# Performance work log

Hardware: AMD Instinct MI355X
Metric: run time of the kernel (lower is better)

The kernel has to match this reference:

```python
import jax, jax.numpy as jnp
import numpy as np

B, T, C = 2, 2048, 1024
N_HEAD = 16
HEAD_DIM = C // N_HEAD


def setup_inputs() -> dict:
    key = jax.random.key(0)
    ks = jax.random.split(key, 5)
    s = 0.02
    return {
        "x": jax.random.normal(ks[0], (B, T, C), dtype=jnp.float32),
        "Wq": jax.random.normal(ks[1], (C, C), dtype=jnp.float32) * s,
        "bq": jnp.zeros((C,), dtype=jnp.float32),
        "Wk": jax.random.normal(ks[2], (C, C), dtype=jnp.float32) * s,
        "bk": jnp.zeros((C,), dtype=jnp.float32),
        "Wv": jax.random.normal(ks[3], (C, C), dtype=jnp.float32) * s,
        "bv": jnp.zeros((C,), dtype=jnp.float32),
        "Wo": jax.random.normal(ks[4], (C, C), dtype=jnp.float32) * s,
        "bo": jnp.zeros((C,), dtype=jnp.float32),
    }


def reference(x, Wq, bq, Wk, bk, Wv, bv, Wo, bo):
    b, t, c = x.shape
    h, d = N_HEAD, HEAD_DIM
    # projections -> [B, H, T, D]
    def proj(W, bias):
        return (x @ W.T + bias).reshape(b, t, h, d).transpose(0, 2, 1, 3)
    q = proj(Wq, bq)
    k = proj(Wk, bk)
    v = proj(Wv, bv)
    att = jnp.einsum("bhqd,bhkd->bhqk", q, k) / jnp.sqrt(jnp.float32(d))
    causal = jnp.tril(jnp.ones((t, t), dtype=bool))
    att = jnp.where(causal, att, jnp.float32(-jnp.inf))
    att = jax.nn.softmax(att, axis=-1)
    y = jnp.einsum("bhqk,bhkd->bhqd", att, v)  # [B,H,T,D]
    y = y.transpose(0, 2, 1, 3).reshape(b, t, c)
    return y @ Wo.T + bo
```

## Files before the change

kernel.cpp:

```cpp
#include <hip/hip_runtime.h>
#include <hip/hip_bf16.h>


namespace {

constexpr int TT = 2048;
constexpr int CC = 1024;
constexpr int HH = 16;
constexpr int DD = 64;

using bf16x8 = __attribute__((ext_vector_type(8))) __bf16;
using bf16x4 = __attribute__((ext_vector_type(4))) __bf16;
using f32x4  = __attribute__((ext_vector_type(4))) float;
using us8    = __attribute__((ext_vector_type(8))) unsigned short;

__device__ __forceinline__ unsigned short f2b(float f) {
  unsigned u = __float_as_uint(f);
  u += 0x7fffu + ((u >> 16) & 1u);
  return (unsigned short)(u >> 16);
}

__device__ __forceinline__ void gload16(const void* g, void* l) {
  __builtin_amdgcn_global_load_lds(
      (const __attribute__((address_space(1))) void*)g,
      (__attribute__((address_space(3))) void*)l, 16, 0, 0);
}

#if __has_builtin(__builtin_amdgcn_exp2f)
#define FEXP2 __builtin_amdgcn_exp2f
#else
#define FEXP2 exp2f
#endif

#define SCALE2 0.18033688011112042f

}

__global__ void k_cvt_all(const float* __restrict__ x,
                          const float* __restrict__ wq, const float* __restrict__ wk,
                          const float* __restrict__ wv, const float* __restrict__ wo,
                          unsigned short* __restrict__ dst) {
  const int i = blockIdx.x * 256 + threadIdx.x;
  const float* src; int off;
  if (i < 1048576)      { src = x;  off = i; }
  else if (i < 1310720) { src = wq; off = i - 1048576; }
  else if (i < 1572864) { src = wk; off = i - 1310720; }
  else if (i < 1835008) { src = wv; off = i - 1572864; }
  else                  { src = wo; off = i - 1835008; }
  float4 v = reinterpret_cast<const float4*>(src)[off];
  ushort4 o;
  o.x = f2b(v.x); o.y = f2b(v.y); o.z = f2b(v.z); o.w = f2b(v.w);
  reinterpret_cast<ushort4*>(dst)[i] = o;
}

__global__ __launch_bounds__(256, 3) void k_gemm_qkv(
    const unsigned short* __restrict__ A,
    const unsigned short* __restrict__ Wq,
    const unsigned short* __restrict__ Wk,
    const unsigned short* __restrict__ Wv,
    const float* __restrict__ bq,
    const float* __restrict__ bk,
    const float* __restrict__ bv,
    unsigned short* __restrict__ qd,
    unsigned short* __restrict__ kd,
    unsigned short* __restrict__ vd)
{
  __shared__ unsigned short la[2][128 * 32];
  __shared__ unsigned short lb[2][128 * 32];
  const int tid = threadIdx.x;
  const int lane = tid & 63;
  const int wid = tid >> 6;
  const int l15 = lane & 15, lg = lane >> 4;
  const int wm = (wid & 1) * 64, wn = (wid >> 1) * 64;
  const int bm = blockIdx.x;
  const int wsel = blockIdx.y >> 3;
  const int bnl = blockIdx.y & 7;

  const unsigned short* W = (wsel == 0) ? Wq : (wsel == 1) ? Wk : Wv;
  const float* bias = (wsel == 0) ? bq : (wsel == 1) ? bk : bv;

  const int srow = lane >> 2;
  const int sko  = (lane & 3) * 8;

  auto STAGE = [&](int buf, int kt) {
#pragma unroll
    for (int s = 0; s < 2; ++s) {
      const int seg = wid * 2 + s;
      const int row = seg * 16 + srow;
      gload16(&A[(bm * 128 + row) * CC + kt * 32 + sko], &la[buf][seg * 512]);
      gload16(&W[(bnl * 128 + row) * CC + kt * 32 + sko], &lb[buf][seg * 512]);
    }
  };

  f32x4 acc[4][4];
#pragma unroll
  for (int i = 0; i < 4; ++i)
#pragma unroll
    for (int j = 0; j < 4; ++j) acc[i][j] = f32x4{0.f, 0.f, 0.f, 0.f};

  auto COMPUTE = [&](int buf) {
    bf16x8 af[4], bf[4];
#pragma unroll
    for (int mi = 0; mi < 4; ++mi)
      af[mi] = __builtin_bit_cast(bf16x8,
        *reinterpret_cast<const us8*>(&la[buf][(wm + mi * 16 + l15) * 32 + lg * 8]));
#pragma unroll
    for (int ni = 0; ni < 4; ++ni)
      bf[ni] = __builtin_bit_cast(bf16x8,
        *reinterpret_cast<const us8*>(&lb[buf][(wn + ni * 16 + l15) * 32 + lg * 8]));
#pragma unroll
    for (int mi = 0; mi < 4; ++mi)
#pragma unroll
      for (int ni = 0; ni < 4; ++ni)
        acc[mi][ni] = __builtin_amdgcn_mfma_f32_16x16x32_bf16(af[mi], bf[ni], acc[mi][ni], 0, 0, 0);
  };

  STAGE(0, 0);
  STAGE(1, 1);
  int cur = 0;
  for (int kt = 0; kt < CC / 32 - 1; ++kt) {
    asm volatile("s_waitcnt vmcnt(4)" ::: "memory");
    __builtin_amdgcn_s_barrier();
    COMPUTE(cur);
    __builtin_amdgcn_s_barrier();
    if (kt < CC / 32 - 2) STAGE(cur, kt + 2);
    cur ^= 1;
  }
  asm volatile("s_waitcnt vmcnt(0)" ::: "memory");
  __builtin_amdgcn_s_barrier();
  COMPUTE(cur);

#pragma unroll
  for (int ni = 0; ni < 4; ++ni) {
    const int nl = bnl * 128 + wn + ni * 16 + l15;
    const float bvl = bias[nl];
    const int hh = nl >> 6, d = nl & (DD - 1);
#pragma unroll
    for (int mi = 0; mi < 4; ++mi) {
#pragma unroll
      for (int r = 0; r < 4; ++r) {
        const int m = bm * 128 + wm + mi * 16 + lg * 4 + r;
        const unsigned short bb = f2b(acc[mi][ni][r] + bvl);
        const int b = m >> 11, t = m & (TT - 1);
        if (wsel == 0)
          qd[((b * HH + hh) * TT + t) * DD + d] = bb;
        else if (wsel == 1)
          kd[((b * HH + hh) * TT + t) * DD + d] = bb;
        else
          vd[((b * HH + hh) * DD + d) * TT + t] = bb;
      }
    }
  }
}

__global__ __launch_bounds__(256, 2) void k_gemm_o(
    const unsigned short* __restrict__ A,
    const unsigned short* __restrict__ W,
    const float* __restrict__ bias,
    float* __restrict__ out)
{
  __shared__ unsigned short la[2][128 * 32];
  __shared__ unsigned short lb[2][64 * 32];
  const int tid = threadIdx.x;
  const int lane = tid & 63;
  const int wid = tid >> 6;
  const int l15 = lane & 15, lg = lane >> 4;
  const int wm = (wid & 1) * 64, wn = (wid >> 1) * 32;
  const int bm = blockIdx.x, bn = blockIdx.y;

  const int srow = lane >> 2;
  const int sko  = (lane & 3) * 8;

  auto STAGE = [&](int buf, int kt) {
#pragma unroll
    for (int s = 0; s < 2; ++s) {
      const int seg = wid * 2 + s;
      gload16(&A[(bm * 128 + seg * 16 + srow) * CC + kt * 32 + sko], &la[buf][seg * 512]);
    }
    gload16(&W[(bn * 64 + wid * 16 + srow) * CC + kt * 32 + sko], &lb[buf][wid * 512]);
  };

  f32x4 acc[4][2];
#pragma unroll
  for (int i = 0; i < 4; ++i)
#pragma unroll
    for (int j = 0; j < 2; ++j) acc[i][j] = f32x4{0.f, 0.f, 0.f, 0.f};

  auto COMPUTE = [&](int buf) {
    bf16x8 af[4], bf[2];
#pragma unroll
    for (int mi = 0; mi < 4; ++mi)
      af[mi] = __builtin_bit_cast(bf16x8,
        *reinterpret_cast<const us8*>(&la[buf][(wm + mi * 16 + l15) * 32 + lg * 8]));
#pragma unroll
    for (int ni = 0; ni < 2; ++ni)
      bf[ni] = __builtin_bit_cast(bf16x8,
        *reinterpret_cast<const us8*>(&lb[buf][(wn + ni * 16 + l15) * 32 + lg * 8]));
#pragma unroll
    for (int mi = 0; mi < 4; ++mi)
#pragma unroll
      for (int ni = 0; ni < 2; ++ni)
        acc[mi][ni] = __builtin_amdgcn_mfma_f32_16x16x32_bf16(af[mi], bf[ni], acc[mi][ni], 0, 0, 0);
  };

  STAGE(0, 0);
  STAGE(1, 1);
  int cur = 0;
  for (int kt = 0; kt < CC / 32 - 1; ++kt) {
    asm volatile("s_waitcnt vmcnt(3)" ::: "memory");
    __builtin_amdgcn_s_barrier();
    COMPUTE(cur);
    __builtin_amdgcn_s_barrier();
    if (kt < CC / 32 - 2) STAGE(cur, kt + 2);
    cur ^= 1;
  }
  asm volatile("s_waitcnt vmcnt(0)" ::: "memory");
  __builtin_amdgcn_s_barrier();
  COMPUTE(cur);

#pragma unroll
  for (int ni = 0; ni < 2; ++ni) {
    const int n = bn * 64 + wn + ni * 16 + l15;
    const float bvl = bias[n];
#pragma unroll
    for (int mi = 0; mi < 4; ++mi)
#pragma unroll
      for (int r = 0; r < 4; ++r) {
        const int m = bm * 128 + wm + mi * 16 + lg * 4 + r;
        out[m * CC + n] = acc[mi][ni][r] + bvl;
      }
  }
}

__global__ __launch_bounds__(64) void k_attn(
    const unsigned short* __restrict__ Q,
    const unsigned short* __restrict__ K,
    const unsigned short* __restrict__ VT,
    unsigned short* __restrict__ Y)
{
  __shared__ unsigned short pl[2][2][16][80];
  const int lane = threadIdx.x;
  const int l15 = lane & 15, lg = lane >> 4;
  const int wg = blockIdx.x + 32 * blockIdx.y;
  const int swz = (wg & 7) * 128 + (wg >> 3);
  const int p = swz & 31;
  const int bh = swz >> 5;
  const int b = bh >> 4, h = bh & 15;
  const int qb0A = p * 32;
  const int qb0B = (63 - p) * 32;
  const int nktA = (qb0A + 95) >> 6;
  const int nktB = (qb0B + 95) >> 6;

  const unsigned short* Qh = Q + bh * TT * DD;
  const unsigned short* Kh = K + bh * TT * DD;
  const unsigned short* Vh = VT + bh * DD * TT;

  auto ldq = [&](bf16x8 (&qf)[2][2], int qb0) {
#pragma unroll
    for (int qi = 0; qi < 2; ++qi)
#pragma unroll
      for (int kk = 0; kk < 2; ++kk)
        qf[qi][kk] = __builtin_bit_cast(bf16x8,
          *reinterpret_cast<const us8*>(&Qh[(qb0 + qi * 16 + l15) * DD + kk * 32 + lg * 8]));
  };
  auto ldk = [&](bf16x8 (&kf)[4][2], int kb) {
#pragma unroll
    for (int f = 0; f < 4; ++f)
#pragma unroll
      for (int kk = 0; kk < 2; ++kk)
        kf[f][kk] = __builtin_bit_cast(bf16x8,
          *reinterpret_cast<const us8*>(&Kh[(kb + f * 16 + l15) * DD + kk * 32 + lg * 8]));
  };
  auto ldv = [&](bf16x8 (&vf)[2][4], int kb) {
#pragma unroll
    for (int kk = 0; kk < 2; ++kk)
#pragma unroll
      for (int dc = 0; dc < 4; ++dc)
        vf[kk][dc] = __builtin_bit_cast(bf16x8,
          *reinterpret_cast<const us8*>(&Vh[(dc * 16 + l15) * TT + kb + kk * 32 + lg * 8]));
  };

  bf16x8 qfA[2][2], qfB[2][2];
  ldq(qfA, qb0A); ldq(qfB, qb0B);

  f32x4 oA[2][4], oB[2][4];
  float mrA[2], lrA[2], mrB[2], lrB[2];
#pragma unroll
  for (int qi = 0; qi < 2; ++qi) {
    mrA[qi] = -INFINITY; lrA[qi] = 0.f;
    mrB[qi] = -INFINITY; lrB[qi] = 0.f;
#pragma unroll
    for (int dc = 0; dc < 4; ++dc) {
      oA[qi][dc] = f32x4{0.f, 0.f, 0.f, 0.f};
      oB[qi][dc] = f32x4{0.f, 0.f, 0.f, 0.f};
    }
  }

  auto processSet = [&](const int qb0, const bf16x8 (&qf)[2][2], f32x4 (&o)[2][4],
                        float (&mr)[2], float (&lr)[2],
                        unsigned short (&plS)[2][16][80],
                        const bf16x8 (&kf)[4][2], const bf16x8 (&vf)[2][4],
                        const int kbase) {
    f32x4 s[2][4];
#pragma unroll
    for (int qi = 0; qi < 2; ++qi)
#pragma unroll
      for (int f = 0; f < 4; ++f) {
        f32x4 t0 = __builtin_amdgcn_mfma_f32_16x16x32_bf16(kf[f][0], qf[qi][0],
                                                           f32x4{0.f,0.f,0.f,0.f}, 0, 0, 0);
        s[qi][f] = __builtin_amdgcn_mfma_f32_16x16x32_bf16(kf[f][1], qf[qi][1], t0, 0, 0, 0);
      }
    const bool needMask = (kbase + 63 > qb0);
#pragma unroll
    for (int qi = 0; qi < 2; ++qi) {
      const int qg = qb0 + qi * 16 + l15;
      float sv[4][4];
      float mt = -INFINITY;
#pragma unroll
      for (int f = 0; f < 4; ++f)
#pragma unroll
        for (int r = 0; r < 4; ++r) {
          float v = s[qi][f][r] * SCALE2;
          if (needMask) v = (kbase + f * 16 + lg * 4 + r <= qg) ? v : -INFINITY;
          sv[f][r] = v;
          mt = fmaxf(mt, v);
        }
      mt = fmaxf(mt, __shfl_xor(mt, 16));
      mt = fmaxf(mt, __shfl_xor(mt, 32));
      const float mn = fmaxf(mr[qi], mt);
      const float al = FEXP2(mr[qi] - mn);
      mr[qi] = mn;
      float rs = 0.f;
#pragma unroll
      for (int f = 0; f < 4; ++f) {
        const float p0 = FEXP2(sv[f][0] - mn), p1 = FEXP2(sv[f][1] - mn);
        const float p2 = FEXP2(sv[f][2] - mn), p3 = FEXP2(sv[f][3] - mn);
        rs += (p0 + p1) + (p2 + p3);
        bf16x4 pk;
        pk[0] = (__bf16)p0; pk[1] = (__bf16)p1; pk[2] = (__bf16)p2; pk[3] = (__bf16)p3;
        *reinterpret_cast<bf16x4*>(&plS[qi][l15][f * 16 + lg * 4]) = pk;
      }
      rs += __shfl_xor(rs, 16);
      rs += __shfl_xor(rs, 32);
      lr[qi] = lr[qi] * al + rs;
      float alr[4];
#pragma unroll
      for (int r = 0; r < 4; ++r) alr[r] = __shfl(al, lg * 4 + r);
#pragma unroll
      for (int dc = 0; dc < 4; ++dc)
#pragma unroll
        for (int r = 0; r < 4; ++r) o[qi][dc][r] *= alr[r];
    }
    asm volatile("s_waitcnt lgkmcnt(0)" ::: "memory");
    __builtin_amdgcn_sched_barrier(0);
#pragma unroll
    for (int qi = 0; qi < 2; ++qi) {
      const bf16x8 pa0 = __builtin_bit_cast(bf16x8,
        *reinterpret_cast<const us8*>(&plS[qi][l15][lg * 8]));
      const bf16x8 pa1 = __builtin_bit_cast(bf16x8,
        *reinterpret_cast<const us8*>(&plS[qi][l15][32 + lg * 8]));
#pragma unroll
      for (int dc = 0; dc < 4; ++dc) {
        o[qi][dc] = __builtin_amdgcn_mfma_f32_16x16x32_bf16(pa0, vf[0][dc], o[qi][dc], 0, 0, 0);
        o[qi][dc] = __builtin_amdgcn_mfma_f32_16x16x32_bf16(pa1, vf[1][dc], o[qi][dc], 0, 0, 0);
      }
    }
  };

  bf16x8 kf0[4][2], kf1[4][2];
  ldk(kf0, 0);
  for (int kt = 0; kt < nktB; kt += 2) {
    bf16x8 vf0[2][4];
    ldv(vf0, kt * 64);
    const int nx1 = (kt + 1 < nktB) ? kt + 1 : nktB - 1;
    ldk(kf1, nx1 * 64);
    processSet(qb0B, qfB, oB, mrB, lrB, pl[0], kf0, vf0, kt * 64);
    if (kt < nktA)
      processSet(qb0A, qfA, oA, mrA, lrA, pl[1], kf0, vf0, kt * 64);
    if (kt + 1 < nktB) {
      bf16x8 vf1[2][4];
      ldv(vf1, (kt + 1) * 64);
      const int nx2 = (kt + 2 < nktB) ? kt + 2 : nktB - 1;
      ldk(kf0, nx2 * 64);
      processSet(qb0B, qfB, oB, mrB, lrB, pl[0], kf1, vf1, (kt + 1) * 64);
      if (kt + 1 < nktA)
        processSet(qb0A, qfA, oA, mrA, lrA, pl[1], kf1, vf1, (kt + 1) * 64);
    }
  }

  auto epi = [&](int qb0, f32x4 (&o)[2][4], float (&lr)[2]) {
#pragma unroll
    for (int qi = 0; qi < 2; ++qi) {
      float linv[4];
#pragma unroll
      for (int r = 0; r < 4; ++r) linv[r] = 1.f / __shfl(lr[qi], lg * 4 + r);
#pragma unroll
      for (int r = 0; r < 4; ++r) {
        const int t = qb0 + qi * 16 + lg * 4 + r;
#pragma unroll
        for (int dc = 0; dc < 4; ++dc)
          Y[(b * TT + t) * CC + h * DD + dc * 16 + l15] = f2b(o[qi][dc][r] * linv[r]);
      }
    }
  };
  epi(qb0B, oB, lrB);
  epi(qb0A, oA, lrA);
}

extern "C" void kernel_launch(void* const* d_in, const int* in_sizes, int n_in,
                              void* d_out, int out_size, void* d_ws, size_t ws_size,
                              hipStream_t stream) {
  const float* x  = (const float*)d_in[0];
  const float* Wq = (const float*)d_in[1];
  const float* bq = (const float*)d_in[2];
  const float* Wk = (const float*)d_in[3];
  const float* bk = (const float*)d_in[4];
  const float* Wv = (const float*)d_in[5];
  const float* bv = (const float*)d_in[6];
  const float* Wo = (const float*)d_in[7];
  const float* bo = (const float*)d_in[8];
  float* out = (float*)d_out;

  unsigned short* ws  = (unsigned short*)d_ws;
  unsigned short* xb  = ws;
  unsigned short* wqb = xb  + 4194304;
  unsigned short* wkb = wqb + 1048576;
  unsigned short* wvb = wkb + 1048576;
  unsigned short* wob = wvb + 1048576;
  unsigned short* qb  = wob + 1048576;
  unsigned short* kb  = qb  + 4194304;
  unsigned short* vt  = kb  + 4194304;
  unsigned short* yb  = xb;

  k_cvt_all<<<8192, 256, 0, stream>>>(x, Wq, Wk, Wv, Wo, ws);

  k_gemm_qkv<<<dim3(32, 24), 256, 0, stream>>>(xb, wqb, wkb, wvb, bq, bk, bv, qb, kb, vt);

  k_attn<<<dim3(32, 32), 64, 0, stream>>>(qb, kb, vt, yb);

  k_gemm_o<<<dim3(32, 16), 256, 0, stream>>>(yb, wob, bo, out);
}
```

Measured before the change: 205.3 us.

## Fold softmax scale into Q projection and transpose PV MFMA operand order

Folds the attention scale into the Q projection epilogue, so the per-score multiply in the softmax is gone. Swaps the operands of the P·V MFMA so the output accumulator is laid out with the query row per lane. This removes the shuffles that broadcast alpha and l, and lets the epilogue write packed bf16x4 stores. It also drops the manual double-buffered K prefetch in favour of a simple per-tile load loop, which may expose more global-load latency.

```diff
diff --git a/kernel.cpp b/kernel.cpp
--- a/kernel.cpp
+++ b/kernel.cpp
@@ -140,7 +140,9 @@
 #pragma unroll
       for (int r = 0; r < 4; ++r) {
         const int m = bm * 128 + wm + mi * 16 + lg * 4 + r;
-        const unsigned short bb = f2b(acc[mi][ni][r] + bvl);
+        float val = acc[mi][ni][r] + bvl;
+        if (wsel == 0) val *= SCALE2;
+        const unsigned short bb = f2b(val);
         const int b = m >> 11, t = m & (TT - 1);
         if (wsel == 0)
           qd[((b * HH + hh) * TT + t) * DD + d] = bb;
@@ -263,22 +265,6 @@
         qf[qi][kk] = __builtin_bit_cast(bf16x8,
           *reinterpret_cast<const us8*>(&Qh[(qb0 + qi * 16 + l15) * DD + kk * 32 + lg * 8]));
   };
-  auto ldk = [&](bf16x8 (&kf)[4][2], int kb) {
-#pragma unroll
-    for (int f = 0; f < 4; ++f)
-#pragma unroll
-      for (int kk = 0; kk < 2; ++kk)
-        kf[f][kk] = __builtin_bit_cast(bf16x8,
-          *reinterpret_cast<const us8*>(&Kh[(kb + f * 16 + l15) * DD + kk * 32 + lg * 8]));
-  };
-  auto ldv = [&](bf16x8 (&vf)[2][4], int kb) {
-#pragma unroll
-    for (int kk = 0; kk < 2; ++kk)
-#pragma unroll
-      for (int dc = 0; dc < 4; ++dc)
-        vf[kk][dc] = __builtin_bit_cast(bf16x8,
-          *reinterpret_cast<const us8*>(&Vh[(dc * 16 + l15) * TT + kb + kk * 32 + lg * 8]));
-  };
 
   bf16x8 qfA[2][2], qfB[2][2];
   ldq(qfA, qb0A); ldq(qfB, qb0B);
@@ -296,110 +282,112 @@
     }
   }
 
-  auto processSet = [&](const int qb0, const bf16x8 (&qf)[2][2], f32x4 (&o)[2][4],
-                        float (&mr)[2], float (&lr)[2],
-                        unsigned short (&plS)[2][16][80],
-                        const bf16x8 (&kf)[4][2], const bf16x8 (&vf)[2][4],
-                        const int kbase) {
-    f32x4 s[2][4];
-#pragma unroll
-    for (int qi = 0; qi < 2; ++qi)
-#pragma unroll
-      for (int f = 0; f < 4; ++f) {
-        f32x4 t0 = __builtin_amdgcn_mfma_f32_16x16x32_bf16(kf[f][0], qf[qi][0],
-                                                           f32x4{0.f,0.f,0.f,0.f}, 0, 0, 0);
-        s[qi][f] = __builtin_amdgcn_mfma_f32_16x16x32_bf16(kf[f][1], qf[qi][1], t0, 0, 0, 0);
+  for (int kt = 0; kt < nktB; ++kt) {
+    const int kbase = kt * 64;
+    bf16x8 kf[4][2], vf[2][4];
+#pragma unroll
+    for (int f = 0; f < 4; ++f)
+#pragma unroll
+      for (int kk = 0; kk < 2; ++kk)
+        kf[f][kk] = __builtin_bit_cast(bf16x8,
+          *reinterpret_cast<const us8*>(&Kh[(kbase + f * 16 + l15) * DD + kk * 32 + lg * 8]));
+#pragma unroll
+    for (int kk = 0; kk < 2; ++kk)
+#pragma unroll
+      for (int dc = 0; dc < 4; ++dc)
+        vf[kk][dc] = __builtin_bit_cast(bf16x8,
+          *reinterpret_cast<const us8*>(&Vh[(dc * 16 + l15) * TT + kbase + kk * 32 + lg * 8]));
+
+    const bool doA = (kt < nktA);
+
+    auto qk_sm = [&](const bf16x8 (&qf)[2][2], const int qb0, float (&mr)[2],
+                     float (&lr)[2], f32x4 (&o)[2][4],
+                     unsigned short (&plS)[2][16][80]) {
+      f32x4 s[2][4];
+#pragma unroll
+      for (int qi = 0; qi < 2; ++qi)
+#pragma unroll
+        for (int f = 0; f < 4; ++f) {
+          f32x4 t0 = __builtin_amdgcn_mfma_f32_16x16x32_bf16(kf[f][0], qf[qi][0],
+                                                             f32x4{0.f,0.f,0.f,0.f}, 0, 0, 0);
+          s[qi][f] = __builtin_amdgcn_mfma_f32_16x16x32_bf16(kf[f][1], qf[qi][1], t0, 0, 0, 0);
+        }
+      const bool needMask = (kbase + 63 > qb0);
+#pragma unroll
+      for (int qi = 0; qi < 2; ++qi) {
+        const int qg = qb0 + qi * 16 + l15;
+        float mt = -INFINITY;
+#pragma unroll
+        for (int f = 0; f < 4; ++f)
+#pragma unroll
+          for (int r = 0; r < 4; ++r) {
+            float v = s[qi][f][r];
+            if (needMask) v = (kbase + f * 16 + lg * 4 + r <= qg) ? v : -INFINITY;
+            s[qi][f][r] = v;
+            mt = fmaxf(mt, v);
+          }
+        mt = fmaxf(mt, __shfl_xor(mt, 16));
+        mt = fmaxf(mt, __shfl_xor(mt, 32));
+        const float mn = fmaxf(mr[qi], mt);
+        const float al = FEXP2(mr[qi] - mn);
+        mr[qi] = mn;
+        float rs = 0.f;
+#pragma unroll
+        for (int f = 0; f < 4; ++f) {
+          const float p0 = FEXP2(s[qi][f][0] - mn), p1 = FEXP2(s[qi][f][1] - mn);
+          const float p2 = FEXP2(s[qi][f][2] - mn), p3 = FEXP2(s[qi][f][3] - mn);
+          rs += (p0 + p1) + (p2 + p3);
+          bf16x4 pk;
+          pk[0] = (__bf16)p0; pk[1] = (__bf16)p1; pk[2] = (__bf16)p2; pk[3] = (__bf16)p3;
+          *reinterpret_cast<bf16x4*>(&plS[qi][l15][f * 16 + lg * 4]) = pk;
+        }
+        rs += __shfl_xor(rs, 16);
+        rs += __shfl_xor(rs, 32);
+        lr[qi] = lr[qi] * al + rs;
+#pragma unroll
+        for (int dc = 0; dc < 4; ++dc)
+#pragma unroll
+          for (int r = 0; r < 4; ++r) o[qi][dc][r] *= al;
       }
-    const bool needMask = (kbase + 63 > qb0);
-#pragma unroll
-    for (int qi = 0; qi < 2; ++qi) {
-      const int qg = qb0 + qi * 16 + l15;
-      float sv[4][4];
-      float mt = -INFINITY;
-#pragma unroll
-      for (int f = 0; f < 4; ++f)
-#pragma unroll
-        for (int r = 0; r < 4; ++r) {
-          float v = s[qi][f][r] * SCALE2;
-          if (needMask) v = (kbase + f * 16 + lg * 4 + r <= qg) ? v : -INFINITY;
-          sv[f][r] = v;
-          mt = fmaxf(mt, v);
-        }
-      mt = fmaxf(mt, __shfl_xor(mt, 16));
-      mt = fmaxf(mt, __shfl_xor(mt, 32));
-      const float mn = fmaxf(mr[qi], mt);
-      const float al = FEXP2(mr[qi] - mn);
-      mr[qi] = mn;
-      float rs = 0.f;
-#pragma unroll
-      for (int f = 0; f < 4; ++f) {
-        const float p0 = FEXP2(sv[f][0] - mn), p1 = FEXP2(sv[f][1] - mn);
-        const float p2 = FEXP2(sv[f][2] - mn), p3 = FEXP2(sv[f][3] - mn);
-        rs += (p0 + p1) + (p2 + p3);
-        bf16x4 pk;
-        pk[0] = (__bf16)p0; pk[1] = (__bf16)p1; pk[2] = (__bf16)p2; pk[3] = (__bf16)p3;
-        *reinterpret_cast<bf16x4*>(&plS[qi][l15][f * 16 + lg * 4]) = pk;
-      }
-      rs += __shfl_xor(rs, 16);
-      rs += __shfl_xor(rs, 32);
-      lr[qi] = lr[qi] * al + rs;
-      float alr[4];
-#pragma unroll
-      for (int r = 0; r < 4; ++r) alr[r] = __shfl(al, lg * 4 + r);
-#pragma unroll
-      for (int dc = 0; dc < 4; ++dc)
-#pragma unroll
-        for (int r = 0; r < 4; ++r) o[qi][dc][r] *= alr[r];
-    }
+    };
+
+    qk_sm(qfB, qb0B, mrB, lrB, oB, pl[0]);
+    if (doA) qk_sm(qfA, qb0A, mrA, lrA, oA, pl[1]);
+
     asm volatile("s_waitcnt lgkmcnt(0)" ::: "memory");
     __builtin_amdgcn_sched_barrier(0);
+
+    auto pv = [&](f32x4 (&o)[2][4], unsigned short (&plS)[2][16][80]) {
+#pragma unroll
+      for (int qi = 0; qi < 2; ++qi) {
+        const bf16x8 pa0 = __builtin_bit_cast(bf16x8,
+          *reinterpret_cast<const us8*>(&plS[qi][l15][lg * 8]));
+        const bf16x8 pa1 = __builtin_bit_cast(bf16x8,
+          *reinterpret_cast<const us8*>(&plS[qi][l15][32 + lg * 8]));
+#pragma unroll
+        for (int dc = 0; dc < 4; ++dc) {
+          o[qi][dc] = __builtin_amdgcn_mfma_f32_16x16x32_bf16(vf[0][dc], pa0, o[qi][dc], 0, 0, 0);
+          o[qi][dc] = __builtin_amdgcn_mfma_f32_16x16x32_bf16(vf[1][dc], pa1, o[qi][dc], 0, 0, 0);
+        }
+      }
+    };
+    pv(oB, pl[0]);
+    if (doA) pv(oA, pl[1]);
+  }
+
+  auto epi = [&](int qb0, f32x4 (&o)[2][4], float (&lr)[2]) {
 #pragma unroll
     for (int qi = 0; qi < 2; ++qi) {
-      const bf16x8 pa0 = __builtin_bit_cast(bf16x8,
-        *reinterpret_cast<const us8*>(&plS[qi][l15][lg * 8]));
-      const bf16x8 pa1 = __builtin_bit_cast(bf16x8,
-        *reinterpret_cast<const us8*>(&plS[qi][l15][32 + lg * 8]));
+      const float linv = 1.f / lr[qi];
+      const int t = qb0 + qi * 16 + l15;
 #pragma unroll
       for (int dc = 0; dc < 4; ++dc) {
-        o[qi][dc] = __builtin_amdgcn_mfma_f32_16x16x32_bf16(pa0, vf[0][dc], o[qi][dc], 0, 0, 0);
-        o[qi][dc] = __builtin_amdgcn_mfma_f32_16x16x32_bf16(pa1, vf[1][dc], o[qi][dc], 0, 0, 0);
-      }
-    }
-  };
-
-  bf16x8 kf0[4][2], kf1[4][2];
-  ldk(kf0, 0);
-  for (int kt = 0; kt < nktB; kt += 2) {
-    bf16x8 vf0[2][4];
-    ldv(vf0, kt * 64);
-    const int nx1 = (kt + 1 < nktB) ? kt + 1 : nktB - 1;
-    ldk(kf1, nx1 * 64);
-    processSet(qb0B, qfB, oB, mrB, lrB, pl[0], kf0, vf0, kt * 64);
-    if (kt < nktA)
-      processSet(qb0A, qfA, oA, mrA, lrA, pl[1], kf0, vf0, kt * 64);
-    if (kt + 1 < nktB) {
-      bf16x8 vf1[2][4];
-      ldv(vf1, (kt + 1) * 64);
-      const int nx2 = (kt + 2 < nktB) ? kt + 2 : nktB - 1;
-      ldk(kf0, nx2 * 64);
-      processSet(qb0B, qfB, oB, mrB, lrB, pl[0], kf1, vf1, (kt + 1) * 64);
-      if (kt + 1 < nktA)
-        processSet(qb0A, qfA, oA, mrA, lrA, pl[1], kf1, vf1, (kt + 1) * 64);
-    }
-  }
-
-  auto epi = [&](int qb0, f32x4 (&o)[2][4], float (&lr)[2]) {
-#pragma unroll
-    for (int qi = 0; qi < 2; ++qi) {
-      float linv[4];
-#pragma unroll
-      for (int r = 0; r < 4; ++r) linv[r] = 1.f / __shfl(lr[qi], lg * 4 + r);
-#pragma unroll
-      for (int r = 0; r < 4; ++r) {
-        const int t = qb0 + qi * 16 + lg * 4 + r;
-#pragma unroll
-        for (int dc = 0; dc < 4; ++dc)
-          Y[(b * TT + t) * CC + h * DD + dc * 16 + l15] = f2b(o[qi][dc][r] * linv[r]);
+        bf16x4 pk;
+#pragma unroll
+        for (int r = 0; r < 4; ++r)
+          pk[r] = __builtin_bit_cast(__bf16, f2b(o[qi][dc][r] * linv));
+        *reinterpret_cast<bf16x4*>(
+            &Y[(b * TT + t) * CC + h * DD + dc * 16 + lg * 4]) = pk;
       }
     }
   };
```

Measured after the change: 210.3 us. 1.02x slower.
